# Kernel optimization log

Hardware: AMD Instinct MI355X
Metric: run time of the kernel (lower is better)

The kernel has to match this reference:

```python
import jax, jax.numpy as jnp
import numpy as np

N, E, B = 10000, 160000, 256
IN, DESC = 57, 1217
# (in_dim, heads, out_per_head) for the 4 GATConv layers
CONV_DIMS = [(57, 5, 114), (570, 5, 171), (855, 5, 114), (570, 1, 570)]
FC_DIMS = [(1024 + DESC, 1024), (1024, 2048), (2048, 1024), (1024, 256), (256, 1)]


def setup_inputs() -> dict:
    key = jax.random.key(0)
    cnt = [0]
    def p(shape, scale=0.05):
        cnt[0] += 1
        return jax.random.normal(jax.random.fold_in(key, cnt[0]), shape, jnp.float32) * scale
    d = {}
    d["x"] = jax.random.normal(jax.random.fold_in(key, 100), (N, IN), jnp.float32)
    d["edge_index"] = jax.random.randint(jax.random.fold_in(key, 101), (2, E), 0, N)
    d["batch"] = jnp.sort(jax.random.randint(jax.random.fold_in(key, 102), (N,), 0, B))
    d["desc"] = jax.random.normal(jax.random.fold_in(key, 103), (B, DESC), jnp.float32)
    for i, (ci, H, C) in enumerate(CONV_DIMS, 1):
        d[f"W{i}"] = p((ci, H * C))
        d[f"as{i}"] = p((H, C))
        d[f"ad{i}"] = p((H, C))
        d[f"b{i}"] = jnp.zeros((H * C,), jnp.float32)
    d["Wg"] = p((570, 1024)); d["bg"] = jnp.zeros((1024,), jnp.float32)
    for i, (ci, co) in enumerate(FC_DIMS, 1):
        d[f"Wf{i}"] = p((ci, co))
        d[f"bf{i}"] = jnp.zeros((co,), jnp.float32)
    return d


def gat_conv(x, src, dst, W, a_src, a_dst, b):
    """PyG GATConv (eval mode: attention dropout off), self-loops already in src/dst."""
    n = x.shape[0]
    H, C = a_src.shape
    h = (x @ W).reshape(n, H, C)                      # [N,H,C]
    al_s = (h * a_src).sum(-1)                         # [N,H]
    al_d = (h * a_dst).sum(-1)                         # [N,H]
    e = jax.nn.leaky_relu(al_s[src] + al_d[dst], 0.2)  # [E,H]
    # segment softmax over destination node
    m = jax.ops.segment_max(e, dst, num_segments=n)
    e = jnp.exp(e - m[dst])
    s = jax.ops.segment_sum(e, dst, num_segments=n)
    alpha = e / (s[dst] + 1e-16)                       # [E,H]
    msg = h[src] * alpha[:, :, None]                   # [E,H,C]
    out = jax.ops.segment_sum(msg, dst, num_segments=n)
    return out.reshape(n, H * C) + b


def reference(x, edge_index, batch, desc,
              W1, as1, ad1, b1, W2, as2, ad2, b2,
              W3, as3, ad3, b3, W4, as4, ad4, b4,
              Wg, bg, Wf1, bf1, Wf2, bf2, Wf3, bf3, Wf4, bf4, Wf5, bf5):
    n = x.shape[0]
    loops = jnp.arange(n)
    src = jnp.concatenate([edge_index[0], loops])
    dst = jnp.concatenate([edge_index[1], loops])
    h = x
    for W, a_s, a_d, b in [(W1, as1, ad1, b1), (W2, as2, ad2, b2),
                           (W3, as3, ad3, b3), (W4, as4, ad4, b4)]:
        h = jax.nn.relu(gat_conv(h, src, dst, W, a_s, a_d, b))
    pooled = jax.ops.segment_sum(h, batch, num_segments=B)   # global_add_pool [B,570]
    g = pooled @ Wg + bg
    z = jnp.concatenate([g, desc], axis=1)                    # [B, 2241]
    z = jax.nn.relu(z @ Wf1 + bf1)
    z = jax.nn.relu(z @ Wf2 + bf2)
    z = jax.nn.relu(z @ Wf3 + bf3)
    z = jax.nn.relu(z @ Wf4 + bf4)
    return z @ Wf5 + bf5                                      # [B,1]
```

## Files before the change

### kernel.cpp

```cpp
#include <hip/hip_runtime.h>
#include <hip/hip_bf16.h>
#include <math.h>

#define NNODES 10000
#define NEDGES 160000
#define NB     256
#define ETOT   (NEDGES + NNODES)
#define INDIM  57
#define DESCD  1217

static inline size_t align256(size_t x) { return (x + 255) & ~size_t(255); }

typedef _Float16 half8_t __attribute__((ext_vector_type(8)));
typedef float f32x4 __attribute__((ext_vector_type(4)));

__device__ inline float wave_max(float v) {
#pragma unroll
  for (int o = 32; o > 0; o >>= 1) v = fmaxf(v, __shfl_xor(v, o));
  return v;
}
__device__ inline float wave_sum(float v) {
#pragma unroll
  for (int o = 32; o > 0; o >>= 1) v += __shfl_xor(v, o);
  return v;
}

__global__ void count_kernel(const int* __restrict__ ei, int* __restrict__ deg) {
  int e = blockIdx.x * blockDim.x + threadIdx.x;
  if (e < ETOT) {
    int dst = (e < NEDGES) ? ei[NEDGES + e] : (e - NEDGES);
    atomicAdd(&deg[dst], 1);
  }
}

__global__ __launch_bounds__(1024) void scan_kernel(const int* __restrict__ deg,
                                                    int* __restrict__ row_ptr,
                                                    int* __restrict__ cursor) {
  __shared__ int part[1024];
  const int CHUNK = (NNODES + 1023) / 1024;
  int t = threadIdx.x;
  int start = t * CHUNK;
  int sum = 0;
  for (int i = 0; i < CHUNK; ++i) {
    int idx = start + i;
    if (idx < NNODES) sum += deg[idx];
  }
  part[t] = sum;
  __syncthreads();
  for (int off = 1; off < 1024; off <<= 1) {
    int v = (t >= off) ? part[t - off] : 0;
    __syncthreads();
    part[t] += v;
    __syncthreads();
  }
  int run = (t > 0) ? part[t - 1] : 0;
  for (int i = 0; i < CHUNK; ++i) {
    int idx = start + i;
    if (idx < NNODES) {
      row_ptr[idx] = run;
      cursor[idx] = run;
      run += deg[idx];
    }
  }
  if (t == 1023) row_ptr[NNODES] = ETOT;
}

__global__ void scatter_kernel(const int* __restrict__ ei, int* __restrict__ cursor,
                               int* __restrict__ csr_src) {
  int e = blockIdx.x * blockDim.x + threadIdx.x;
  if (e < ETOT) {
    int src, dst;
    if (e < NEDGES) { src = ei[e]; dst = ei[NEDGES + e]; }
    else            { src = e - NEDGES; dst = src; }
    int idx = atomicAdd(&cursor[dst], 1);
    csr_src[idx] = src;
  }
}

__global__ void convert_x_kernel(const float* __restrict__ x, _Float16* __restrict__ x16) {
  int t = blockIdx.x * blockDim.x + threadIdx.x;
  if (t >= NNODES * 64) return;
  int n = t >> 6, k = t & 63;
  x16[t] = (_Float16)((k < INDIM) ? x[n * INDIM + k] : 0.f);
}

struct TMat { const float* src; _Float16* dst; int K, N, Kpad, tiles_k, tile_base; };
struct TParams { TMat m[9]; };

__global__ __launch_bounds__(256) void transpose_w_kernel(TParams P, int nm) {
  __shared__ float tile[64][65];
  int bt = blockIdx.x;
  int mi = 0;
#pragma unroll
  for (int i = 1; i < 9; ++i)
    if (i < nm && bt >= P.m[i].tile_base) mi = i;
  TMat m = P.m[mi];
  int lt = bt - m.tile_base;
  int tk = lt % m.tiles_k, tn = lt / m.tiles_k;
  int k0 = tk * 64, n0 = tn * 64;
  int c = threadIdx.x & 63, r4 = threadIdx.x >> 6;
#pragma unroll
  for (int i = 0; i < 16; ++i) {
    int kr = r4 + i * 4;
    int gk = k0 + kr, gn = n0 + c;
    tile[kr][c] = (gk < m.K && gn < m.N) ? m.src[(size_t)gk * m.N + gn] : 0.f;
  }
  __syncthreads();
#pragma unroll
  for (int i = 0; i < 16; ++i) {
    int nr = r4 + i * 4;
    int gn = n0 + nr, gk = k0 + c;
    if (gn < m.N && gk < m.K)
      m.dst[(size_t)gn * m.Kpad + gk] = (_Float16)tile[c][nr];
  }
}

struct LMat { const float* W; const float* as; const float* ad; _Float16* dst;
              int K, HC, C, H, Kpad, la, wave_base; };

__global__ __launch_bounds__(256) void logitw_kernel(LMat m0, LMat m1, LMat m2, LMat m3,
                                                     int nwaves) {
  int gw = (blockIdx.x * 256 + threadIdx.x) >> 6;
  int lane = threadIdx.x & 63;
  if (gw >= nwaves) return;
  LMat m = m3;
  if (gw < m1.wave_base) m = m0;
  else if (gw < m2.wave_base) m = m1;
  else if (gw < m3.wave_base) m = m2;
  int li = gw - m.wave_base;
  int H2 = 2 * m.H;
  int k = li / H2, r = li - k * H2;
  int h = (r >= m.H) ? r - m.H : r;
  const float* a = (r >= m.H) ? m.ad : m.as;
  float s = 0.f;
  for (int c = lane; c < m.C; c += 64)
    s += m.W[(size_t)k * m.HC + h * m.C + c] * a[h * m.C + c];
  s = wave_sum(s);
  if (lane == 0) m.dst[(size_t)(m.la + r) * m.Kpad + k] = (_Float16)s;
}

__global__ void pooled16_kernel(const float* __restrict__ pooled, _Float16* __restrict__ p16) {
  int t = blockIdx.x * blockDim.x + threadIdx.x;
  if (t >= NB * 576) return;
  int b = t / 576, c = t - b * 576;
  p16[t] = (_Float16)((c < 570) ? pooled[b * 570 + c] : 0.f);
}

__global__ void desc_fill_kernel(const float* __restrict__ desc, _Float16* __restrict__ z16) {
  int t = blockIdx.x * blockDim.x + threadIdx.x;
  if (t >= NB * 1280) return;
  int b = t / 1280, i = t - b * 1280;
  z16[(size_t)b * 2304 + 1024 + i] = (_Float16)((i < DESCD) ? desc[b * DESCD + i] : 0.f);
}

__global__ __launch_bounds__(256) void mfma_gemm_kernel(
    const _Float16* __restrict__ A, const _Float16* __restrict__ Bt,
    _Float16* __restrict__ C, int M, int Kpad, int Nreal, int ldc) {
  __shared__ __align__(16) char smem[32768];
  char* AsB = smem;
  char* BsB = smem + 16384;
  int tid = threadIdx.x;
  int lane = tid & 63, wid = tid >> 6;
  int l15 = lane & 15, g = lane >> 4;
  int wr = wid >> 1, wc = wid & 1;
  int m0 = blockIdx.y * 128, n0 = blockIdx.x * 128;
  f32x4 acc[4][4];
#pragma unroll
  for (int i = 0; i < 4; ++i)
#pragma unroll
    for (int j = 0; j < 4; ++j) acc[i][j] = (f32x4){0.f, 0.f, 0.f, 0.f};

  int KT = Kpad >> 6;
  half8_t pa[4], pb[4];
#pragma unroll
  for (int i = 0; i < 4; ++i) {
    int r = i * 32 + (tid >> 3);
    int cs = (tid & 7) ^ (r & 7);
    int ga = min(m0 + r, M - 1);
    pa[i] = *(const half8_t*)(A + (size_t)ga * Kpad + cs * 8);
    pb[i] = *(const half8_t*)(Bt + (size_t)(n0 + r) * Kpad + cs * 8);
  }
  for (int kt = 0; kt < KT; ++kt) {
    __syncthreads();
#pragma unroll
    for (int i = 0; i < 4; ++i) {
      *(half8_t*)(AsB + i * 4096 + tid * 16) = pa[i];
      *(half8_t*)(BsB + i * 4096 + tid * 16) = pb[i];
    }
    __syncthreads();
    if (kt + 1 < KT) {
      int k0 = (kt + 1) << 6;
#pragma unroll
      for (int i = 0; i < 4; ++i) {
        int r = i * 32 + (tid >> 3);
        int cs = (tid & 7) ^ (r & 7);
        int ga = min(m0 + r, M - 1);
        pa[i] = *(const half8_t*)(A + (size_t)ga * Kpad + k0 + cs * 8);
        pb[i] = *(const half8_t*)(Bt + (size_t)(n0 + r) * Kpad + k0 + cs * 8);
      }
    }
#pragma unroll
    for (int kk = 0; kk < 2; ++kk) {
      half8_t af[4], bf[4];
#pragma unroll
      for (int f = 0; f < 4; ++f) {
        int ra = wr * 64 + f * 16 + l15;
        af[f] = *(const half8_t*)(AsB + ra * 128 + (((kk * 4 + g) ^ (ra & 7)) << 4));
        int cb = wc * 64 + f * 16 + l15;
        bf[f] = *(const half8_t*)(BsB + cb * 128 + (((kk * 4 + g) ^ (cb & 7)) << 4));
      }
#pragma unroll
      for (int fm = 0; fm < 4; ++fm)
#pragma unroll
        for (int fn = 0; fn < 4; ++fn)
          acc[fm][fn] = __builtin_amdgcn_mfma_f32_16x16x32_f16(af[fm], bf[fn], acc[fm][fn], 0, 0, 0);
    }
  }
#pragma unroll
  for (int fm = 0; fm < 4; ++fm) {
    int gmb = m0 + wr * 64 + fm * 16 + g * 4;
#pragma unroll
    for (int fn = 0; fn < 4; ++fn) {
      int gn = n0 + wc * 64 + fn * 16 + l15;
      if (gn >= Nreal) continue;
#pragma unroll
      for (int j = 0; j < 4; ++j) {
        int gm = gmb + j;
        if (gm < M) C[(size_t)gm * ldc + gn] = (_Float16)acc[fm][fn][j];
      }
    }
  }
}

__global__ __launch_bounds__(256) void mfma_splitk_kernel(
    const _Float16* __restrict__ A, const _Float16* __restrict__ Bt,
    float* __restrict__ P, int M, int Kpad, int N, int ktpc) {
  __shared__ __align__(16) char smem[32768];
  char* AsB = smem;
  char* BsB = smem + 16384;
  int tid = threadIdx.x;
  int lane = tid & 63, wid = tid >> 6;
  int l15 = lane & 15, g = lane >> 4;
  int wr = wid >> 1, wc = wid & 1;
  int m0 = blockIdx.y * 128, n0 = blockIdx.x * 128;
  int z = blockIdx.z;
  int KT = Kpad >> 6;
  int ktb = z * ktpc;
  int kte = min(KT, ktb + ktpc);
  f32x4 acc[4][4];
#pragma unroll
  for (int i = 0; i < 4; ++i)
#pragma unroll
    for (int j = 0; j < 4; ++j) acc[i][j] = (f32x4){0.f, 0.f, 0.f, 0.f};

  half8_t pa[4], pb[4];
  {
    int k0 = ktb << 6;
#pragma unroll
    for (int i = 0; i < 4; ++i) {
      int r = i * 32 + (tid >> 3);
      int cs = (tid & 7) ^ (r & 7);
      int ga = min(m0 + r, M - 1);
      pa[i] = *(const half8_t*)(A + (size_t)ga * Kpad + k0 + cs * 8);
      pb[i] = *(const half8_t*)(Bt + (size_t)(n0 + r) * Kpad + k0 + cs * 8);
    }
  }
  for (int kt = ktb; kt < kte; ++kt) {
    __syncthreads();
#pragma unroll
    for (int i = 0; i < 4; ++i) {
      *(half8_t*)(AsB + i * 4096 + tid * 16) = pa[i];
      *(half8_t*)(BsB + i * 4096 + tid * 16) = pb[i];
    }
    __syncthreads();
    if (kt + 1 < kte) {
      int k0 = (kt + 1) << 6;
#pragma unroll
      for (int i = 0; i < 4; ++i) {
        int r = i * 32 + (tid >> 3);
        int cs = (tid & 7) ^ (r & 7);
        int ga = min(m0 + r, M - 1);
        pa[i] = *(const half8_t*)(A + (size_t)ga * Kpad + k0 + cs * 8);
        pb[i] = *(const half8_t*)(Bt + (size_t)(n0 + r) * Kpad + k0 + cs * 8);
      }
    }
#pragma unroll
    for (int kk = 0; kk < 2; ++kk) {
      half8_t af[4], bf[4];
#pragma unroll
      for (int f = 0; f < 4; ++f) {
        int ra = wr * 64 + f * 16 + l15;
        af[f] = *(const half8_t*)(AsB + ra * 128 + (((kk * 4 + g) ^ (ra & 7)) << 4));
        int cb = wc * 64 + f * 16 + l15;
        bf[f] = *(const half8_t*)(BsB + cb * 128 + (((kk * 4 + g) ^ (cb & 7)) << 4));
      }
#pragma unroll
      for (int fm = 0; fm < 4; ++fm)
#pragma unroll
        for (int fn = 0; fn < 4; ++fn)
          acc[fm][fn] = __builtin_amdgcn_mfma_f32_16x16x32_f16(af[fm], bf[fn], acc[fm][fn], 0, 0, 0);
    }
  }
  size_t zb = (size_t)z * M;
#pragma unroll
  for (int fm = 0; fm < 4; ++fm) {
    int gmb = m0 + wr * 64 + fm * 16 + g * 4;
#pragma unroll
    for (int fn = 0; fn < 4; ++fn) {
      int gn = n0 + wc * 64 + fn * 16 + l15;
      if (gn >= N) continue;
#pragma unroll
      for (int j = 0; j < 4; ++j) {
        int gm = gmb + j;
        if (gm < M) P[(zb + gm) * N + gn] = acc[fm][fn][j];
      }
    }
  }
}

__global__ void reduce16_kernel(const float* __restrict__ P, const float* __restrict__ bias,
                                _Float16* __restrict__ O, int M, int N, int ldo,
                                int S, int relu) {
  int idx = blockIdx.x * blockDim.x + threadIdx.x;
  if (idx >= M * ldo) return;
  int row = idx / ldo, col = idx - row * ldo;
  if (col >= N) return;
  float s = bias[col];
  int MN = M * N;
  for (int z = 0; z < S; ++z) s += P[(size_t)z * MN + row * N + col];
  if (relu) s = fmaxf(s, 0.f);
  O[idx] = (_Float16)s;
}

__global__ __launch_bounds__(256) void fc5_kernel(const _Float16* __restrict__ A,
                                                  const float* __restrict__ w,
                                                  const float* __restrict__ b,
                                                  float* __restrict__ out) {
  int wid = threadIdx.x >> 6, lane = threadIdx.x & 63;
  int m = blockIdx.x * 4 + wid;
  if (m >= NB) return;
  float s = 0.f;
  for (int k = lane; k < 256; k += 64) s += (float)A[m * 256 + k] * w[k];
  s = wave_sum(s);
  if (lane == 0) out[m] = s + b[0];
}

template <int H>
__global__ __launch_bounds__(256) void att_kernel_t(const _Float16* __restrict__ hbuf,
                                                    int ldh, int la,
                                                    const int* __restrict__ row_ptr,
                                                    const int* __restrict__ csr_src,
                                                    float* __restrict__ alpha_t) {
  int wid = threadIdx.x >> 6, lane = threadIdx.x & 63;
  int n = blockIdx.x * 4 + wid;
  if (n >= NNODES) return;
  int rp = row_ptr[n], deg = row_ptr[n + 1] - rp;
  float ad[H], m[H], e0[H], e1[H], ssum[H];
#pragma unroll
  for (int h = 0; h < H; ++h) {
    ad[h] = (float)hbuf[(size_t)n * ldh + la + H + h];
    m[h] = -1e30f; ssum[h] = 0.f;
  }
  for (int j = lane, it = 0; j < deg; j += 64, ++it) {
    int s = csr_src[rp + j];
    half8_t v = *(const half8_t*)(hbuf + (size_t)s * ldh + la);
#pragma unroll
    for (int h = 0; h < H; ++h) {
      float e = (float)v[h] + ad[h];
      e = (e >= 0.f) ? e : 0.2f * e;
      if (it == 0) e0[h] = e; else if (it == 1) e1[h] = e;
      m[h] = fmaxf(m[h], e);
    }
  }
#pragma unroll
  for (int h = 0; h < H; ++h) m[h] = wave_max(m[h]);
  for (int j = lane, it = 0; j < deg; j += 64, ++it) {
    half8_t v{};
    if (it >= 2) v = *(const half8_t*)(hbuf + (size_t)csr_src[rp + j] * ldh + la);
#pragma unroll
    for (int h = 0; h < H; ++h) {
      float e;
      if (it == 0) e = e0[h];
      else if (it == 1) e = e1[h];
      else { e = (float)v[h] + ad[h]; e = (e >= 0.f) ? e : 0.2f * e; }
      ssum[h] += expf(e - m[h]);
    }
  }
#pragma unroll
  for (int h = 0; h < H; ++h) ssum[h] = 1.f / (wave_sum(ssum[h]) + 1e-16f);
  for (int j = lane, it = 0; j < deg; j += 64, ++it) {
    half8_t v{};
    if (it >= 2) v = *(const half8_t*)(hbuf + (size_t)csr_src[rp + j] * ldh + la);
#pragma unroll
    for (int h = 0; h < H; ++h) {
      float e;
      if (it == 0) e = e0[h];
      else if (it == 1) e = e1[h];
      else { e = (float)v[h] + ad[h]; e = (e >= 0.f) ? e : 0.2f * e; }
      alpha_t[(size_t)h * ETOT + rp + j] = expf(e - m[h]) * ssum[h];
    }
  }
}

__global__ __launch_bounds__(256) void agg_kernel(const _Float16* __restrict__ hbuf,
                                                  const float* __restrict__ alpha_t,
                                                  const int* __restrict__ row_ptr,
                                                  const int* __restrict__ csr_src,
                                                  const float* __restrict__ bias,
                                                  _Float16* __restrict__ h16o,
                                                  int H, int C, int ldh, int ldo,
                                                  int HC, int nchunks) {
  int wid = threadIdx.x >> 6, lane = threadIdx.x & 63;
  int gw = blockIdx.x * 4 + wid;
  int n = gw / nchunks, chunk = gw - n * nchunks;
  if (n >= NNODES) return;
  int k0 = chunk * 512 + lane * 8;
  if (k0 >= ldo) return;
  _Float16* op = h16o + (size_t)n * ldo + k0;
  if (k0 >= HC) { *(half8_t*)op = (half8_t){}; return; }
  int h0 = k0 / C;
  int h1 = min(k0 + 7, HC - 1) / C;
  int split = (h0 + 1) * C;
  const float* A0 = alpha_t + (size_t)h0 * ETOT;
  const float* A1 = alpha_t + (size_t)h1 * ETOT;
  int rp = row_ptr[n], re = row_ptr[n + 1];
  float acc[8] = {};
  int j = rp;
  for (; j < re && (j & 3); ++j) {
    int s = csr_src[j];
    float a0 = A0[j], a1 = A1[j];
    half8_t v = *(const half8_t*)(hbuf + (size_t)s * ldh + k0);
#pragma unroll
    for (int i = 0; i < 8; ++i) acc[i] += ((k0 + i < split) ? a0 : a1) * (float)v[i];
  }
  for (; j + 4 <= re; j += 4) {
    int4 s4 = *(const int4*)(csr_src + j);
    float4 a0v = *(const float4*)(A0 + j);
    float4 a1v = *(const float4*)(A1 + j);
    half8_t v0 = *(const half8_t*)(hbuf + (size_t)s4.x * ldh + k0);
    half8_t v1 = *(const half8_t*)(hbuf + (size_t)s4.y * ldh + k0);
    half8_t v2 = *(const half8_t*)(hbuf + (size_t)s4.z * ldh + k0);
    half8_t v3 = *(const half8_t*)(hbuf + (size_t)s4.w * ldh + k0);
#pragma unroll
    for (int i = 0; i < 8; ++i) {
      bool lo = (k0 + i < split);
      float a = lo ? a0v.x : a1v.x;
      float b = lo ? a0v.y : a1v.y;
      float c = lo ? a0v.z : a1v.z;
      float d = lo ? a0v.w : a1v.w;
      acc[i] += a * (float)v0[i] + b * (float)v1[i];
      acc[i] += c * (float)v2[i] + d * (float)v3[i];
    }
  }
  for (; j < re; ++j) {
    int s = csr_src[j];
    float a0 = A0[j], a1 = A1[j];
    half8_t v = *(const half8_t*)(hbuf + (size_t)s * ldh + k0);
#pragma unroll
    for (int i = 0; i < 8; ++i) acc[i] += ((k0 + i < split) ? a0 : a1) * (float)v[i];
  }
  half8_t o;
#pragma unroll
  for (int i = 0; i < 8; ++i)
    o[i] = (_Float16)((k0 + i < HC) ? fmaxf(acc[i] + bias[k0 + i], 0.f) : 0.f);
  *(half8_t*)op = o;
}

__global__ __launch_bounds__(256) void pool_kernel(const _Float16* __restrict__ h4,
                                                   const int* __restrict__ batch,
                                                   float* __restrict__ pooled, int F, int ldh) {
  int wid = threadIdx.x >> 6, lane = threadIdx.x & 63;
  int n = blockIdx.x * 4 + wid;
  if (n >= NNODES) return;
  int b = batch[n];
  for (int k = lane; k < F; k += 64)
    atomicAdd(&pooled[(size_t)b * F + k], (float)h4[(size_t)n * ldh + k]);
}

extern "C" void kernel_launch(void* const* d_in, const int* in_sizes, int n_in,
                              void* d_out, int out_size, void* d_ws, size_t ws_size,
                              hipStream_t stream) {
  const float* x    = (const float*)d_in[0];
  const int*   ei   = (const int*)d_in[1];
  const int*   batch= (const int*)d_in[2];
  const float* desc = (const float*)d_in[3];
  const float* W1 = (const float*)d_in[4];  const float* as1 = (const float*)d_in[5];
  const float* ad1 = (const float*)d_in[6]; const float* b1 = (const float*)d_in[7];
  const float* W2 = (const float*)d_in[8];  const float* as2 = (const float*)d_in[9];
  const float* ad2 = (const float*)d_in[10];const float* b2 = (const float*)d_in[11];
  const float* W3 = (const float*)d_in[12]; const float* as3 = (const float*)d_in[13];
  const float* ad3 = (const float*)d_in[14];const float* b3 = (const float*)d_in[15];
  const float* W4 = (const float*)d_in[16]; const float* as4 = (const float*)d_in[17];
  const float* ad4 = (const float*)d_in[18];const float* b4 = (const float*)d_in[19];
  const float* Wg = (const float*)d_in[20]; const float* bg = (const float*)d_in[21];
  const float* Wf1 = (const float*)d_in[22];const float* bf1 = (const float*)d_in[23];
  const float* Wf2 = (const float*)d_in[24];const float* bf2 = (const float*)d_in[25];
  const float* Wf3 = (const float*)d_in[26];const float* bf3 = (const float*)d_in[27];
  const float* Wf4 = (const float*)d_in[28];const float* bf4 = (const float*)d_in[29];
  const float* Wf5 = (const float*)d_in[30];const float* bf5 = (const float*)d_in[31];
  float* out = (float*)d_out;

  char* p = (char*)d_ws;
  size_t off = 0;
  auto alloc = [&](size_t bytes) -> char* {
    char* r = p + off;
    off = align256(off + bytes);
    return r;
  };
  int*      deg     = (int*)alloc(sizeof(int) * NNODES);
  int*      row_ptr = (int*)alloc(sizeof(int) * (NNODES + 1));
  int*      cursor  = (int*)alloc(sizeof(int) * NNODES);
  int*      csr_src = (int*)alloc(sizeof(int) * ETOT);
  float*    alpha_t = (float*)alloc(sizeof(float) * (size_t)5 * ETOT);
  _Float16* x16     = (_Float16*)alloc(sizeof(_Float16) * (size_t)NNODES * 64);
  _Float16* hA16    = (_Float16*)alloc(sizeof(_Float16) * ((size_t)NNODES * 872 + 1024));
  _Float16* h16     = (_Float16*)alloc(sizeof(_Float16) * ((size_t)NNODES * 896 + 1024));
  size_t wt_begin = off;
  _Float16* WtL1 = (_Float16*)alloc(sizeof(_Float16) * 640 * 64);
  _Float16* WtL2 = (_Float16*)alloc(sizeof(_Float16) * 896 * 576);
  _Float16* WtL3 = (_Float16*)alloc(sizeof(_Float16) * 640 * 896);
  _Float16* WtL4 = (_Float16*)alloc(sizeof(_Float16) * 640 * 576);
  _Float16* WtG  = (_Float16*)alloc(sizeof(_Float16) * 1024 * 576);
  _Float16* WtF1 = (_Float16*)alloc(sizeof(_Float16) * 1024 * 2304);
  _Float16* WtF2 = (_Float16*)alloc(sizeof(_Float16) * 2048 * 1024);
  _Float16* WtF3 = (_Float16*)alloc(sizeof(_Float16) * 1024 * 2048);
  _Float16* WtF4 = (_Float16*)alloc(sizeof(_Float16) * 256 * 1024);
  size_t wt_end = off;
  float*    pooled  = (float*)alloc(sizeof(float) * NB * 570);
  _Float16* p16     = (_Float16*)alloc(sizeof(_Float16) * NB * 576);
  _Float16* z16     = (_Float16*)alloc(sizeof(_Float16) * NB * 2304);
  _Float16* t16     = (_Float16*)alloc(sizeof(_Float16) * NB * 2048);
  _Float16* u16     = (_Float16*)alloc(sizeof(_Float16) * NB * 2048);
  _Float16* v16     = (_Float16*)alloc(sizeof(_Float16) * NB * 256);
  (void)ws_size;

  hipMemsetAsync(deg, 0, sizeof(int) * NNODES, stream);
  {
    dim3 g((ETOT + 255) / 256);
    count_kernel<<<g, 256, 0, stream>>>(ei, deg);
    scan_kernel<<<1, 1024, 0, stream>>>(deg, row_ptr, cursor);
    scatter_kernel<<<g, 256, 0, stream>>>(ei, cursor, csr_src);
  }
  convert_x_kernel<<<(NNODES * 64 + 255) / 256, 256, 0, stream>>>(x, x16);

  hipMemsetAsync(p + wt_begin, 0, wt_end - wt_begin, stream);
  {
    auto tiles = [](int K, int N) { return ((K + 63) / 64) * ((N + 63) / 64); };
    TParams tp;
    int base = 0;
    auto add = [&](int i, const float* src, _Float16* dst, int K, int N, int Kpad) {
      tp.m[i] = { src, dst, K, N, Kpad, (K + 63) / 64, base };
      base += tiles(K, N);
    };
    add(0, W1,  WtL1, INDIM,        570,   64);
    add(1, W2,  WtL2, 570,          855,  576);
    add(2, W3,  WtL3, 855,          570,  896);
    add(3, W4,  WtL4, 570,          570,  576);
    add(4, Wg,  WtG,  570,          1024,  576);
    add(5, Wf1, WtF1, 1024 + DESCD, 1024, 2304);
    add(6, Wf2, WtF2, 1024,         2048, 1024);
    add(7, Wf3, WtF3, 2048,         1024, 2048);
    add(8, Wf4, WtF4, 1024,          256, 1024);
    transpose_w_kernel<<<base, 256, 0, stream>>>(tp, 9);
  }
  {
    LMat m0 = { W1, as1, ad1, WtL1, INDIM, 570, 114, 5,  64, 576, 0 };
    LMat m1 = { W2, as2, ad2, WtL2, 570,   855, 171, 5, 576, 856, INDIM * 10 };
    LMat m2 = { W3, as3, ad3, WtL3, 855,   570, 114, 5, 896, 576, INDIM * 10 + 5700 };
    LMat m3 = { W4, as4, ad4, WtL4, 570,   570, 570, 1, 576, 576, INDIM * 10 + 5700 + 8550 };
    int nwaves = INDIM * 10 + 5700 + 8550 + 1140;
    logitw_kernel<<<(nwaves * 64 + 255) / 256, 256, 0, stream>>>(m0, m1, m2, m3, nwaves);
  }

  dim3 gnode((NNODES + 3) / 4);

  struct LayerDef { _Float16* Wt; const float* b;
                    int H, C, HC, Kpad, Npad, ldh, la, ldo; };
  LayerDef L[4] = {
    { WtL1, b1, 5, 114, 570,  64, 640, 592, 576, 576 },
    { WtL2, b2, 5, 171, 855, 576, 896, 872, 856, 896 },
    { WtL3, b3, 5, 114, 570, 896, 640, 592, 576, 576 },
    { WtL4, b4, 1, 570, 570, 576, 640, 592, 576, 576 },
  };
  for (int l = 0; l < 4; ++l) {
    int Nreal = L[l].la + 2 * L[l].H;
    {
      const _Float16* Ain = (l == 0) ? x16 : h16;
      dim3 g(L[l].Npad / 128, (NNODES + 127) / 128);
      mfma_gemm_kernel<<<g, 256, 0, stream>>>(Ain, L[l].Wt, hA16, NNODES, L[l].Kpad,
                                              Nreal, L[l].ldh);
    }
    if (L[l].H == 5)
      att_kernel_t<5><<<gnode, 256, 0, stream>>>(hA16, L[l].ldh, L[l].la,
                                                 row_ptr, csr_src, alpha_t);
    else
      att_kernel_t<1><<<gnode, 256, 0, stream>>>(hA16, L[l].ldh, L[l].la,
                                                 row_ptr, csr_src, alpha_t);
    {
      int nchunks = (L[l].ldo + 511) / 512;
      dim3 g((NNODES * nchunks + 3) / 4);
      agg_kernel<<<g, 256, 0, stream>>>(hA16, alpha_t, row_ptr, csr_src, L[l].b, h16,
                                        L[l].H, L[l].C, L[l].ldh, L[l].ldo, L[l].HC, nchunks);
    }
  }

  hipMemsetAsync(pooled, 0, sizeof(float) * NB * 570, stream);
  pool_kernel<<<gnode, 256, 0, stream>>>(h16, batch, pooled, 570, 576);

  float* partials = (float*)hA16;
  auto head_gemm = [&](const _Float16* A, const _Float16* Wt, const float* bias,
                       _Float16* O, int Kpad, int N, int ldo, int relu,
                       int ktpc, int S) {
    dim3 g(N / 128, NB / 128, S);
    mfma_splitk_kernel<<<g, 256, 0, stream>>>(A, Wt, partials, NB, Kpad, N, ktpc);
    int totO = NB * ldo;
    reduce16_kernel<<<(totO + 255) / 256, 256, 0, stream>>>(partials, bias, O, NB, N, ldo, S, relu);
  };

  pooled16_kernel<<<(NB * 576 + 255) / 256, 256, 0, stream>>>(pooled, p16);
  head_gemm(p16, WtG, bg, z16, 576, 1024, 2304, 0, 3, 3);
  desc_fill_kernel<<<(NB * 1280 + 255) / 256, 256, 0, stream>>>(desc, z16);
  head_gemm(z16, WtF1, bf1, t16, 2304, 1024, 1024, 1, 3, 12);
  head_gemm(t16, WtF2, bf2, u16, 1024, 2048, 2048, 1, 2, 8);
  head_gemm(u16, WtF3, bf3, t16, 2048, 1024, 1024, 1, 2, 16);
  head_gemm(t16, WtF4, bf4, v16, 1024,  256,  256, 1, 1, 16);
  fc5_kernel<<<(NB + 3) / 4, 256, 0, stream>>>(v16, Wf5, bf5, out);
}
```

Measured before the change: 474.9 us.

## Pad per-head channels to multiples of 8, store alpha in fp16, fp16 aggregation

Lays out each head's channels padded to a multiple of 8 (114→120, 171→176) in the GEMM weights and hidden buffers, so every 8-wide vector in the aggregation belongs to a single head and the two-alpha select goes away. Attention coefficients are stored as fp16 instead of fp32, halving alpha traffic. The aggregation now accumulates in packed half2 arithmetic with an 8-edge unrolled loop. The padding adds some GEMM width and larger buffers, and fp16 accumulation over high-degree nodes may lose precision.

```diff
diff --git a/kernel.cpp b/kernel.cpp
--- a/kernel.cpp
+++ b/kernel.cpp
@@ -12,6 +12,8 @@
 static inline size_t align256(size_t x) { return (x + 255) & ~size_t(255); }
 
 typedef _Float16 half8_t __attribute__((ext_vector_type(8)));
+typedef _Float16 half4v_t __attribute__((ext_vector_type(4)));
+typedef _Float16 half2_t __attribute__((ext_vector_type(2)));
 typedef float f32x4 __attribute__((ext_vector_type(4)));
 
 __device__ inline float wave_max(float v) {
@@ -84,7 +86,8 @@
   x16[t] = (_Float16)((k < INDIM) ? x[n * INDIM + k] : 0.f);
 }
 
-struct TMat { const float* src; _Float16* dst; int K, N, Kpad, tiles_k, tile_base; };
+struct TMat { const float* src; _Float16* dst; int K, N, Kpad, tiles_k, tile_base;
+              int Cn, Cnp, Ck, Ckp; };
 struct TParams { TMat m[9]; };
 
 __global__ __launch_bounds__(256) void transpose_w_kernel(TParams P, int nm) {
@@ -110,13 +113,16 @@
   for (int i = 0; i < 16; ++i) {
     int nr = r4 + i * 4;
     int gn = n0 + nr, gk = k0 + c;
-    if (gn < m.N && gk < m.K)
-      m.dst[(size_t)gn * m.Kpad + gk] = (_Float16)tile[c][nr];
+    if (gn < m.N && gk < m.K) {
+      int np = gn + (gn / m.Cn) * (m.Cnp - m.Cn);
+      int kp = gk + (gk / m.Ck) * (m.Ckp - m.Ck);
+      m.dst[(size_t)np * m.Kpad + kp] = (_Float16)tile[c][nr];
+    }
   }
 }
 
 struct LMat { const float* W; const float* as; const float* ad; _Float16* dst;
-              int K, HC, C, H, Kpad, la, wave_base; };
+              int K, HC, C, H, Kpad, la, wave_base, Ck, Ckp; };
 
 __global__ __launch_bounds__(256) void logitw_kernel(LMat m0, LMat m1, LMat m2, LMat m3,
                                                      int nwaves) {
@@ -136,7 +142,8 @@
   for (int c = lane; c < m.C; c += 64)
     s += m.W[(size_t)k * m.HC + h * m.C + c] * a[h * m.C + c];
   s = wave_sum(s);
-  if (lane == 0) m.dst[(size_t)(m.la + r) * m.Kpad + k] = (_Float16)s;
+  int kp = k + (k / m.Ck) * (m.Ckp - m.Ck);
+  if (lane == 0) m.dst[(size_t)(m.la + r) * m.Kpad + kp] = (_Float16)s;
 }
 
 __global__ void pooled16_kernel(const float* __restrict__ pooled, _Float16* __restrict__ p16) {
@@ -350,7 +357,7 @@
                                                     int ldh, int la,
                                                     const int* __restrict__ row_ptr,
                                                     const int* __restrict__ csr_src,
-                                                    float* __restrict__ alpha_t) {
+                                                    _Float16* __restrict__ alpha_t) {
   int wid = threadIdx.x >> 6, lane = threadIdx.x & 63;
   int n = blockIdx.x * 4 + wid;
   if (n >= NNODES) return;
@@ -397,19 +404,19 @@
       if (it == 0) e = e0[h];
       else if (it == 1) e = e1[h];
       else { e = (float)v[h] + ad[h]; e = (e >= 0.f) ? e : 0.2f * e; }
-      alpha_t[(size_t)h * ETOT + rp + j] = expf(e - m[h]) * ssum[h];
+      alpha_t[(size_t)h * ETOT + rp + j] = (_Float16)(expf(e - m[h]) * ssum[h]);
     }
   }
 }
 
 __global__ __launch_bounds__(256) void agg_kernel(const _Float16* __restrict__ hbuf,
-                                                  const float* __restrict__ alpha_t,
+                                                  const _Float16* __restrict__ alpha_t,
                                                   const int* __restrict__ row_ptr,
                                                   const int* __restrict__ csr_src,
                                                   const float* __restrict__ bias,
                                                   _Float16* __restrict__ h16o,
-                                                  int H, int C, int ldh, int ldo,
-                                                  int HC, int nchunks) {
+                                                  int C, int Cpad, int ldh, int ldo,
+                                                  int HCpad, int nchunks) {
   int wid = threadIdx.x >> 6, lane = threadIdx.x & 63;
   int gw = blockIdx.x * 4 + wid;
   int n = gw / nchunks, chunk = gw - n * nchunks;
@@ -417,52 +424,47 @@
   int k0 = chunk * 512 + lane * 8;
   if (k0 >= ldo) return;
   _Float16* op = h16o + (size_t)n * ldo + k0;
-  if (k0 >= HC) { *(half8_t*)op = (half8_t){}; return; }
-  int h0 = k0 / C;
-  int h1 = min(k0 + 7, HC - 1) / C;
-  int split = (h0 + 1) * C;
-  const float* A0 = alpha_t + (size_t)h0 * ETOT;
-  const float* A1 = alpha_t + (size_t)h1 * ETOT;
+  if (k0 >= HCpad) { *(half8_t*)op = (half8_t){}; return; }
+  int h0 = k0 / Cpad;
+  int off = k0 - h0 * Cpad;
+  const _Float16* A0 = alpha_t + (size_t)h0 * ETOT;
+  const _Float16* hb = hbuf + k0;
   int rp = row_ptr[n], re = row_ptr[n + 1];
-  float acc[8] = {};
+  half2_t acc0{}, acc1{}, acc2{}, acc3{};
+  auto step = [&](int s, _Float16 a) {
+    half8_t v = *(const half8_t*)(hb + (size_t)s * ldh);
+    half2_t av{a, a};
+    acc0 += av * half2_t{v[0], v[1]};
+    acc1 += av * half2_t{v[2], v[3]};
+    acc2 += av * half2_t{v[4], v[5]};
+    acc3 += av * half2_t{v[6], v[7]};
+  };
   int j = rp;
-  for (; j < re && (j & 3); ++j) {
-    int s = csr_src[j];
-    float a0 = A0[j], a1 = A1[j];
-    half8_t v = *(const half8_t*)(hbuf + (size_t)s * ldh + k0);
-#pragma unroll
-    for (int i = 0; i < 8; ++i) acc[i] += ((k0 + i < split) ? a0 : a1) * (float)v[i];
+  for (; j < re && (j & 3); ++j) step(csr_src[j], A0[j]);
+  for (; j + 8 <= re; j += 8) {
+    int4 sa = *(const int4*)(csr_src + j);
+    int4 sb = *(const int4*)(csr_src + j + 4);
+    half4v_t aa = *(const half4v_t*)(A0 + j);
+    half4v_t ab = *(const half4v_t*)(A0 + j + 4);
+    step(sa.x, aa[0]); step(sa.y, aa[1]); step(sa.z, aa[2]); step(sa.w, aa[3]);
+    step(sb.x, ab[0]); step(sb.y, ab[1]); step(sb.z, ab[2]); step(sb.w, ab[3]);
   }
   for (; j + 4 <= re; j += 4) {
-    int4 s4 = *(const int4*)(csr_src + j);
-    float4 a0v = *(const float4*)(A0 + j);
-    float4 a1v = *(const float4*)(A1 + j);
-    half8_t v0 = *(const half8_t*)(hbuf + (size_t)s4.x * ldh + k0);
-    half8_t v1 = *(const half8_t*)(hbuf + (size_t)s4.y * ldh + k0);
-    half8_t v2 = *(const half8_t*)(hbuf + (size_t)s4.z * ldh + k0);
-    half8_t v3 = *(const half8_t*)(hbuf + (size_t)s4.w * ldh + k0);
-#pragma unroll
-    for (int i = 0; i < 8; ++i) {
-      bool lo = (k0 + i < split);
-      float a = lo ? a0v.x : a1v.x;
-      float b = lo ? a0v.y : a1v.y;
-      float c = lo ? a0v.z : a1v.z;
-      float d = lo ? a0v.w : a1v.w;
-      acc[i] += a * (float)v0[i] + b * (float)v1[i];
-      acc[i] += c * (float)v2[i] + d * (float)v3[i];
-    }
-  }
-  for (; j < re; ++j) {
-    int s = csr_src[j];
-    float a0 = A0[j], a1 = A1[j];
-    half8_t v = *(const half8_t*)(hbuf + (size_t)s * ldh + k0);
-#pragma unroll
-    for (int i = 0; i < 8; ++i) acc[i] += ((k0 + i < split) ? a0 : a1) * (float)v[i];
-  }
+    int4 sa = *(const int4*)(csr_src + j);
+    half4v_t aa = *(const half4v_t*)(A0 + j);
+    step(sa.x, aa[0]); step(sa.y, aa[1]); step(sa.z, aa[2]); step(sa.w, aa[3]);
+  }
+  for (; j < re; ++j) step(csr_src[j], A0[j]);
+  int base = h0 * C + off;
+  int nreal = C - off;
+  float af[8] = {(float)acc0[0], (float)acc0[1], (float)acc1[0], (float)acc1[1],
+                 (float)acc2[0], (float)acc2[1], (float)acc3[0], (float)acc3[1]};
   half8_t o;
 #pragma unroll
-  for (int i = 0; i < 8; ++i)
-    o[i] = (_Float16)((k0 + i < HC) ? fmaxf(acc[i] + bias[k0 + i], 0.f) : 0.f);
+  for (int i = 0; i < 8; ++i) {
+    float bv = bias[base + ((i < nreal) ? i : 0)];
+    o[i] = (i < nreal) ? (_Float16)fmaxf(af[i] + bv, 0.f) : (_Float16)0.f;
+  }
   *(half8_t*)op = o;
 }
 
@@ -511,15 +513,15 @@
   int*      row_ptr = (int*)alloc(sizeof(int) * (NNODES + 1));
   int*      cursor  = (int*)alloc(sizeof(int) * NNODES);
   int*      csr_src = (int*)alloc(sizeof(int) * ETOT);
-  float*    alpha_t = (float*)alloc(sizeof(float) * (size_t)5 * ETOT);
+  _Float16* alpha_t = (_Float16*)alloc(sizeof(_Float16) * (size_t)5 * ETOT);
   _Float16* x16     = (_Float16*)alloc(sizeof(_Float16) * (size_t)NNODES * 64);
-  _Float16* hA16    = (_Float16*)alloc(sizeof(_Float16) * ((size_t)NNODES * 872 + 1024));
+  _Float16* hA16    = (_Float16*)alloc(sizeof(_Float16) * ((size_t)NNODES * 896 + 1024));
   _Float16* h16     = (_Float16*)alloc(sizeof(_Float16) * ((size_t)NNODES * 896 + 1024));
   size_t wt_begin = off;
   _Float16* WtL1 = (_Float16*)alloc(sizeof(_Float16) * 640 * 64);
-  _Float16* WtL2 = (_Float16*)alloc(sizeof(_Float16) * 896 * 576);
+  _Float16* WtL2 = (_Float16*)alloc(sizeof(_Float16) * 896 * 640);
   _Float16* WtL3 = (_Float16*)alloc(sizeof(_Float16) * 640 * 896);
-  _Float16* WtL4 = (_Float16*)alloc(sizeof(_Float16) * 640 * 576);
+  _Float16* WtL4 = (_Float16*)alloc(sizeof(_Float16) * 640 * 640);
   _Float16* WtG  = (_Float16*)alloc(sizeof(_Float16) * 1024 * 576);
   _Float16* WtF1 = (_Float16*)alloc(sizeof(_Float16) * 1024 * 2304);
   _Float16* WtF2 = (_Float16*)alloc(sizeof(_Float16) * 2048 * 1024);
@@ -548,26 +550,27 @@
     auto tiles = [](int K, int N) { return ((K + 63) / 64) * ((N + 63) / 64); };
     TParams tp;
     int base = 0;
-    auto add = [&](int i, const float* src, _Float16* dst, int K, int N, int Kpad) {
-      tp.m[i] = { src, dst, K, N, Kpad, (K + 63) / 64, base };
+    auto add = [&](int i, const float* src, _Float16* dst, int K, int N, int Kpad,
+                   int Cn, int Cnp, int Ck, int Ckp) {
+      tp.m[i] = { src, dst, K, N, Kpad, (K + 63) / 64, base, Cn, Cnp, Ck, Ckp };
       base += tiles(K, N);
     };
-    add(0, W1,  WtL1, INDIM,        570,   64);
-    add(1, W2,  WtL2, 570,          855,  576);
-    add(2, W3,  WtL3, 855,          570,  896);
-    add(3, W4,  WtL4, 570,          570,  576);
-    add(4, Wg,  WtG,  570,          1024,  576);
-    add(5, Wf1, WtF1, 1024 + DESCD, 1024, 2304);
-    add(6, Wf2, WtF2, 1024,         2048, 1024);
-    add(7, Wf3, WtF3, 2048,         1024, 2048);
-    add(8, Wf4, WtF4, 1024,          256, 1024);
+    add(0, W1,  WtL1, INDIM,        570,   64, 114, 120, INDIM, INDIM);
+    add(1, W2,  WtL2, 570,          855,  640, 171, 176, 114, 120);
+    add(2, W3,  WtL3, 855,          570,  896, 114, 120, 171, 176);
+    add(3, W4,  WtL4, 570,          570,  640, 570, 570, 114, 120);
+    add(4, Wg,  WtG,  570,          1024,  576, 1024, 1024, 570, 570);
+    add(5, Wf1, WtF1, 1024 + DESCD, 1024, 2304, 1024, 1024, 2304, 2304);
+    add(6, Wf2, WtF2, 1024,         2048, 1024, 2048, 2048, 1024, 1024);
+    add(7, Wf3, WtF3, 2048,         1024, 2048, 1024, 1024, 2048, 2048);
+    add(8, Wf4, WtF4, 1024,          256, 1024, 256, 256, 1024, 1024);
     transpose_w_kernel<<<base, 256, 0, stream>>>(tp, 9);
   }
   {
-    LMat m0 = { W1, as1, ad1, WtL1, INDIM, 570, 114, 5,  64, 576, 0 };
-    LMat m1 = { W2, as2, ad2, WtL2, 570,   855, 171, 5, 576, 856, INDIM * 10 };
-    LMat m2 = { W3, as3, ad3, WtL3, 855,   570, 114, 5, 896, 576, INDIM * 10 + 5700 };
-    LMat m3 = { W4, as4, ad4, WtL4, 570,   570, 570, 1, 576, 576, INDIM * 10 + 5700 + 8550 };
+    LMat m0 = { W1, as1, ad1, WtL1, INDIM, 570, 114, 5,  64, 600, 0, INDIM, INDIM };
+    LMat m1 = { W2, as2, ad2, WtL2, 570,   855, 171, 5, 640, 880, INDIM * 10, 114, 120 };
+    LMat m2 = { W3, as3, ad3, WtL3, 855,   570, 114, 5, 896, 600, INDIM * 10 + 5700, 171, 176 };
+    LMat m3 = { W4, as4, ad4, WtL4, 570,   570, 570, 1, 640, 576, INDIM * 10 + 5700 + 8550, 114, 120 };
     int nwaves = INDIM * 10 + 5700 + 8550 + 1140;
     logitw_kernel<<<(nwaves * 64 + 255) / 256, 256, 0, stream>>>(m0, m1, m2, m3, nwaves);
   }
@@ -575,20 +578,19 @@
   dim3 gnode((NNODES + 3) / 4);
 
   struct LayerDef { _Float16* Wt; const float* b;
-                    int H, C, HC, Kpad, Npad, ldh, la, ldo; };
+                    int H, C, Cpad, HCpad, Kpad, Npad, ldh, la, Nreal, ldo; };
   LayerDef L[4] = {
-    { WtL1, b1, 5, 114, 570,  64, 640, 592, 576, 576 },
-    { WtL2, b2, 5, 171, 855, 576, 896, 872, 856, 896 },
-    { WtL3, b3, 5, 114, 570, 896, 640, 592, 576, 576 },
-    { WtL4, b4, 1, 570, 570, 576, 640, 592, 576, 576 },
+    { WtL1, b1, 5, 114, 120, 600,  64, 640, 616, 600, 610, 640 },
+    { WtL2, b2, 5, 171, 176, 880, 640, 896, 896, 880, 890, 896 },
+    { WtL3, b3, 5, 114, 120, 600, 896, 640, 616, 600, 610, 640 },
+    { WtL4, b4, 1, 570, 576, 576, 640, 640, 584, 576, 578, 576 },
   };
   for (int l = 0; l < 4; ++l) {
-    int Nreal = L[l].la + 2 * L[l].H;
     {
       const _Float16* Ain = (l == 0) ? x16 : h16;
       dim3 g(L[l].Npad / 128, (NNODES + 127) / 128);
       mfma_gemm_kernel<<<g, 256, 0, stream>>>(Ain, L[l].Wt, hA16, NNODES, L[l].Kpad,
-                                              Nreal, L[l].ldh);
+                                              L[l].Nreal, L[l].ldh);
     }
     if (L[l].H == 5)
       att_kernel_t<5><<<gnode, 256, 0, stream>>>(hA16, L[l].ldh, L[l].la,
@@ -600,7 +602,8 @@
       int nchunks = (L[l].ldo + 511) / 512;
       dim3 g((NNODES * nchunks + 3) / 4);
       agg_kernel<<<g, 256, 0, stream>>>(hA16, alpha_t, row_ptr, csr_src, L[l].b, h16,
-                                        L[l].H, L[l].C, L[l].ldh, L[l].ldo, L[l].HC, nchunks);
+                                        L[l].C, L[l].Cpad, L[l].ldh, L[l].ldo,
+                                        L[l].HCpad, nchunks);
     }
   }
 
```

Result: faster. 462.2 us (-2.7%).
